# Kernel optimization log

Measured on AMD Instinct MI355X. Metric: run time of the kernel, lower is better.

Reference implementation:

```python
import jax, jax.numpy as jnp
import numpy as np

HIDDEN_DIM = 64
MEMORY_SLOTS = 8
SEQ_LEN = 24
VOCAB_SIZE = 64
B = 262144


def setup_inputs() -> dict:
    key = jax.random.key(0)
    ks = jax.random.split(key, 7)
    return {
        "seqs": jax.random.randint(ks[0], (B, SEQ_LEN), 0, VOCAB_SIZE, dtype=jnp.int64) if jax.config.jax_enable_x64 else jax.random.randint(ks[0], (B, SEQ_LEN), 0, VOCAB_SIZE, dtype=jnp.int32),
        "query_tok": jax.random.randint(ks[1], (B,), 0, VOCAB_SIZE, dtype=jnp.int32),
        "embed_W": jax.random.normal(ks[2], (VOCAB_SIZE + 2, HIDDEN_DIM), dtype=jnp.float32),
        "W1": jax.random.normal(ks[3], (HIDDEN_DIM, 2 * HIDDEN_DIM), dtype=jnp.float32) * 0.08,
        "b1": jax.random.normal(ks[4], (HIDDEN_DIM,), dtype=jnp.float32) * 0.02,
        "W2": jax.random.normal(ks[5], (VOCAB_SIZE, HIDDEN_DIM), dtype=jnp.float32) * 0.12,
        "b2": jax.random.normal(ks[6], (VOCAB_SIZE,), dtype=jnp.float32) * 0.02,
    }


def reference(seqs, query_tok, embed_W, W1, b1, W2, b2):
    # FIFO of size MEMORY_SLOTS over tokens t in [0, SEQ_LEN-1):
    # mem_summary depends only on the last MEMORY_SLOTS of those tokens.
    mem_toks = seqs[:, SEQ_LEN - 1 - MEMORY_SLOTS : SEQ_LEN - 1]      # [B, M]
    mem_summary = jnp.mean(embed_W[mem_toks], axis=1)                 # [B, H]
    q_emb = embed_W[query_tok]                                        # [B, H]
    x = jnp.concatenate([q_emb, mem_summary], axis=-1)               # [B, 2H]
    h = jax.nn.relu(x @ W1.T + b1)                                    # [B, H]
    logits = h @ W2.T + b2                                            # [B, V]
    return logits
```

## Files before the change

kernel.cpp:

```cpp
#include <hip/hip_runtime.h>


#define RSTRIDE_W 36
#define T2_OFF_W  (64 * RSTRIDE_W)
#define LDS_DW    (2 * 64 * RSTRIDE_W)

typedef __attribute__((ext_vector_type(4))) float    f32x4;
typedef __attribute__((ext_vector_type(4))) int      i32x4;
typedef __attribute__((ext_vector_type(8))) _Float16 f16x8;

__global__ void prep_kernel(const float* __restrict__ embed,
                            const float* __restrict__ W1,
                            const float* __restrict__ b1,
                            unsigned short* __restrict__ T) {
  const int t    = blockIdx.x & 63;
  const int half = blockIdx.x >> 6;
  const int j    = threadIdx.x;
  const f32x4* w4 = (const f32x4*)(W1 + j * 128 + half * 64);
  const f32x4* e4 = (const f32x4*)(embed + t * 64);
  float acc = 0.f;
#pragma unroll
  for (int k = 0; k < 16; ++k) {
    f32x4 a = w4[k], b = e4[k];
    acc += a[0] * b[0] + a[1] * b[1] + a[2] * b[2] + a[3] * b[3];
  }
  const float outv = half ? acc * 0.125f : acc + b1[j];
  ((_Float16*)T)[half * (64 * 2 * RSTRIDE_W) + t * (2 * RSTRIDE_W) + j] =
      (_Float16)outv;
}

__global__ __launch_bounds__(256, 4) void lru_kernel(
    const int*      __restrict__ seqs,
    const int*      __restrict__ qtok,
    const float*    __restrict__ W2,
    const float*    __restrict__ b2,
    const unsigned* __restrict__ T,
    float*          __restrict__ out) {
  __shared__ __align__(16) unsigned lds[LDS_DW];
  const int tid = threadIdx.x;

  {
    const uint4* src = (const uint4*)T;
    uint4*       dst = (uint4*)lds;
#pragma unroll
    for (int r = 0; r < 4; ++r) dst[tid + r * 256] = src[tid + r * 256];
    if (tid < 128) dst[tid + 1024] = src[tid + 1024];
  }

  const int lane = tid & 63;
  const int wv   = tid >> 6;
  const int qd   = lane >> 4;
  const int l15  = lane & 15;

  f16x8 bfr[4][2];
  float bb[4];
#pragma unroll
  for (int nt = 0; nt < 4; ++nt) {
    const int    row = l15 * 4 + nt;
    const float* wr  = W2 + row * 64 + qd * 8;
#pragma unroll
    for (int ks = 0; ks < 2; ++ks) {
      f32x4 w0 = *(const f32x4*)(wr + ks * 32);
      f32x4 w1 = *(const f32x4*)(wr + ks * 32 + 4);
      f16x8 f;
      f[0] = (_Float16)w0[0]; f[1] = (_Float16)w0[1];
      f[2] = (_Float16)w0[2]; f[3] = (_Float16)w0[3];
      f[4] = (_Float16)w1[0]; f[5] = (_Float16)w1[1];
      f[6] = (_Float16)w1[2]; f[7] = (_Float16)w1[3];
      bfr[nt][ks] = f;
    }
    bb[nt] = b2[row];
  }

  const int wbase  = blockIdx.x * 256 + wv * 64;
  const int myelem = wbase + lane;
  const int* srow  = seqs + myelem * 24;
  const i32x4 t0 = __builtin_nontemporal_load((const i32x4*)(srow + 12));
  const i32x4 t1 = __builtin_nontemporal_load((const i32x4*)(srow + 16));
  const i32x4 t2 = __builtin_nontemporal_load((const i32x4*)(srow + 20));
  const int   tq = __builtin_nontemporal_load(qtok + myelem);
  __syncthreads();

#pragma unroll
  for (int it = 0; it < 4; ++it) {
    const int b0  = wbase + it * 16;
    const int src = it * 16 + l15;

    const int qt = __shfl(tq, src);
    int tk[8];
    tk[0] = __shfl(t0.w, src);
    tk[1] = __shfl(t1.x, src);
    tk[2] = __shfl(t1.y, src);
    tk[3] = __shfl(t1.z, src);
    tk[4] = __shfl(t1.w, src);
    tk[5] = __shfl(t2.x, src);
    tk[6] = __shfl(t2.y, src);
    tk[7] = __shfl(t2.z, src);

    f16x8 a0, a1;
    {
      const f16x8* r1 = (const f16x8*)(lds + qt * RSTRIDE_W + qd * 4);
      a0 = r1[0];
      a1 = r1[4];
    }
#pragma unroll
    for (int s = 0; s < 8; ++s) {
      const f16x8* r2 =
          (const f16x8*)(lds + T2_OFF_W + tk[s] * RSTRIDE_W + qd * 4);
      a0 += r2[0];
      a1 += r2[4];
    }
    const f16x8 z = {(_Float16)0, (_Float16)0, (_Float16)0, (_Float16)0,
                     (_Float16)0, (_Float16)0, (_Float16)0, (_Float16)0};
    const f16x8 afA = __builtin_elementwise_max(a0, z);
    const f16x8 afB = __builtin_elementwise_max(a1, z);

    f32x4 acc[4];
#pragma unroll
    for (int nt = 0; nt < 4; ++nt) {
      f32x4 a;
      a[0] = bb[nt]; a[1] = bb[nt]; a[2] = bb[nt]; a[3] = bb[nt];
      a = __builtin_amdgcn_mfma_f32_16x16x32_f16(afA, bfr[nt][0], a, 0, 0, 0);
      a = __builtin_amdgcn_mfma_f32_16x16x32_f16(afB, bfr[nt][1], a, 0, 0, 0);
      acc[nt] = a;
    }
    float* op = out + (size_t)(b0 + qd * 4) * 64 + l15 * 4;
#pragma unroll
    for (int r = 0; r < 4; ++r) {
      f32x4 v;
      v[0] = acc[0][r]; v[1] = acc[1][r]; v[2] = acc[2][r]; v[3] = acc[3][r];
      __builtin_nontemporal_store(v, (f32x4*)(op + (size_t)r * 64));
    }
  }
}

extern "C" void kernel_launch(void* const* d_in, const int* in_sizes, int n_in,
                              void* d_out, int out_size, void* d_ws, size_t ws_size,
                              hipStream_t stream) {
  const int*   seqs  = (const int*)d_in[0];
  const int*   qtokp = (const int*)d_in[1];
  const float* embed = (const float*)d_in[2];
  const float* W1    = (const float*)d_in[3];
  const float* b1    = (const float*)d_in[4];
  const float* W2    = (const float*)d_in[5];
  const float* b2    = (const float*)d_in[6];
  float*       outp  = (float*)d_out;

  prep_kernel<<<dim3(128), dim3(64), 0, stream>>>(embed, W1, b1,
                                                  (unsigned short*)d_ws);
  lru_kernel<<<dim3(1024), dim3(256), 0, stream>>>(seqs, qtokp, W2, b2,
                                                   (const unsigned*)d_ws, outp);
}
```

Before: 113.1 us.

## Precompute fp16 W2 fragments in prep kernel and swap MFMA operand roles

Result: slower. 124.5 us (+10.1%).

```diff
diff --git a/kernel.cpp b/kernel.cpp
--- a/kernel.cpp
+++ b/kernel.cpp
@@ -4,6 +4,7 @@
 #define RSTRIDE_W 36
 #define T2_OFF_W  (64 * RSTRIDE_W)
 #define LDS_DW    (2 * 64 * RSTRIDE_W)
+#define W2F_OFF_H (128 * 2 * RSTRIDE_W)
 
 typedef __attribute__((ext_vector_type(4))) float    f32x4;
 typedef __attribute__((ext_vector_type(4))) int      i32x4;
@@ -12,27 +13,45 @@
 __global__ void prep_kernel(const float* __restrict__ embed,
                             const float* __restrict__ W1,
                             const float* __restrict__ b1,
+                            const float* __restrict__ W2,
                             unsigned short* __restrict__ T) {
-  const int t    = blockIdx.x & 63;
-  const int half = blockIdx.x >> 6;
-  const int j    = threadIdx.x;
-  const f32x4* w4 = (const f32x4*)(W1 + j * 128 + half * 64);
-  const f32x4* e4 = (const f32x4*)(embed + t * 64);
-  float acc = 0.f;
+  const int bid = blockIdx.x;
+  const int j   = threadIdx.x;
+  if (bid < 128) {
+    const int t    = bid & 63;
+    const int half = bid >> 6;
+    const f32x4* w4 = (const f32x4*)(W1 + j * 128 + half * 64);
+    const f32x4* e4 = (const f32x4*)(embed + t * 64);
+    float acc = 0.f;
 #pragma unroll
-  for (int k = 0; k < 16; ++k) {
-    f32x4 a = w4[k], b = e4[k];
-    acc += a[0] * b[0] + a[1] * b[1] + a[2] * b[2] + a[3] * b[3];
+    for (int k = 0; k < 16; ++k) {
+      f32x4 a = w4[k], b = e4[k];
+      acc += a[0] * b[0] + a[1] * b[1] + a[2] * b[2] + a[3] * b[3];
+    }
+    const float outv = half ? acc * 0.125f : acc + b1[j];
+    ((_Float16*)T)[half * (64 * 2 * RSTRIDE_W) + t * (2 * RSTRIDE_W) + j] =
+        (_Float16)outv;
+  } else {
+    const int b   = bid - 128;
+    const int nt  = b >> 1;
+    const int ks  = b & 1;
+    const int l15 = j & 15;
+    const int qd  = j >> 4;
+    const float* wr = W2 + (nt * 16 + l15) * 64 + ks * 32 + qd * 8;
+    f32x4 w0 = *(const f32x4*)(wr);
+    f32x4 w1 = *(const f32x4*)(wr + 4);
+    f16x8 f;
+    f[0] = (_Float16)w0[0]; f[1] = (_Float16)w0[1];
+    f[2] = (_Float16)w0[2]; f[3] = (_Float16)w0[3];
+    f[4] = (_Float16)w1[0]; f[5] = (_Float16)w1[1];
+    f[6] = (_Float16)w1[2]; f[7] = (_Float16)w1[3];
+    *(f16x8*)((_Float16*)T + W2F_OFF_H + (size_t)(b * 64 + j) * 8) = f;
   }
-  const float outv = half ? acc * 0.125f : acc + b1[j];
-  ((_Float16*)T)[half * (64 * 2 * RSTRIDE_W) + t * (2 * RSTRIDE_W) + j] =
-      (_Float16)outv;
 }
 
 __global__ __launch_bounds__(256, 4) void lru_kernel(
     const int*      __restrict__ seqs,
     const int*      __restrict__ qtok,
-    const float*    __restrict__ W2,
     const float*    __restrict__ b2,
     const unsigned* __restrict__ T,
     float*          __restrict__ out) {
@@ -52,24 +71,18 @@
   const int qd   = lane >> 4;
   const int l15  = lane & 15;
 
-  f16x8 bfr[4][2];
-  float bb[4];
+  f16x8 afW[4][2];
+  f32x4 bb4[4];
+  {
+    const _Float16* w2f = (const _Float16*)T + W2F_OFF_H;
 #pragma unroll
-  for (int nt = 0; nt < 4; ++nt) {
-    const int    row = l15 * 4 + nt;
-    const float* wr  = W2 + row * 64 + qd * 8;
+    for (int nt = 0; nt < 4; ++nt) {
 #pragma unroll
-    for (int ks = 0; ks < 2; ++ks) {
-      f32x4 w0 = *(const f32x4*)(wr + ks * 32);
-      f32x4 w1 = *(const f32x4*)(wr + ks * 32 + 4);
-      f16x8 f;
-      f[0] = (_Float16)w0[0]; f[1] = (_Float16)w0[1];
-      f[2] = (_Float16)w0[2]; f[3] = (_Float16)w0[3];
-      f[4] = (_Float16)w1[0]; f[5] = (_Float16)w1[1];
-      f[6] = (_Float16)w1[2]; f[7] = (_Float16)w1[3];
-      bfr[nt][ks] = f;
+      for (int ks = 0; ks < 2; ++ks)
+        afW[nt][ks] =
+            *(const f16x8*)(w2f + (size_t)(((nt << 1) | ks) * 64 + lane) * 8);
+      bb4[nt] = *(const f32x4*)(b2 + nt * 16 + qd * 4);
     }
-    bb[nt] = b2[row];
   }
 
   const int wbase  = blockIdx.x * 256 + wv * 64;
@@ -115,21 +128,13 @@
     const f16x8 afA = __builtin_elementwise_max(a0, z);
     const f16x8 afB = __builtin_elementwise_max(a1, z);
 
-    f32x4 acc[4];
+    float* op = out + (size_t)(b0 + l15) * 64 + qd * 4;
 #pragma unroll
     for (int nt = 0; nt < 4; ++nt) {
-      f32x4 a;
-      a[0] = bb[nt]; a[1] = bb[nt]; a[2] = bb[nt]; a[3] = bb[nt];
-      a = __builtin_amdgcn_mfma_f32_16x16x32_f16(afA, bfr[nt][0], a, 0, 0, 0);
-      a = __builtin_amdgcn_mfma_f32_16x16x32_f16(afB, bfr[nt][1], a, 0, 0, 0);
-      acc[nt] = a;
-    }
-    float* op = out + (size_t)(b0 + qd * 4) * 64 + l15 * 4;
-#pragma unroll
-    for (int r = 0; r < 4; ++r) {
-      f32x4 v;
-      v[0] = acc[0][r]; v[1] = acc[1][r]; v[2] = acc[2][r]; v[3] = acc[3][r];
-      __builtin_nontemporal_store(v, (f32x4*)(op + (size_t)r * 64));
+      f32x4 a = bb4[nt];
+      a = __builtin_amdgcn_mfma_f32_16x16x32_f16(afW[nt][0], afA, a, 0, 0, 0);
+      a = __builtin_amdgcn_mfma_f32_16x16x32_f16(afW[nt][1], afB, a, 0, 0, 0);
+      __builtin_nontemporal_store(a, (f32x4*)(op + nt * 16));
     }
   }
 }
@@ -146,8 +151,8 @@
   const float* b2    = (const float*)d_in[6];
   float*       outp  = (float*)d_out;
 
-  prep_kernel<<<dim3(128), dim3(64), 0, stream>>>(embed, W1, b1,
+  prep_kernel<<<dim3(136), dim3(64), 0, stream>>>(embed, W1, b1, W2,
                                                   (unsigned short*)d_ws);
-  lru_kernel<<<dim3(1024), dim3(256), 0, stream>>>(seqs, qtokp, W2, b2,
+  lru_kernel<<<dim3(1024), dim3(256), 0, stream>>>(seqs, qtokp, b2,
                                                    (const unsigned*)d_ws, outp);
 }
```

## Pack memory tokens into bytes, transpose MFMA operands, and widen prep blocks

Applied to the files above, without the earlier changes.

New measurement: 117.4 us. 3.8% more time.

```diff
diff --git a/kernel.cpp b/kernel.cpp
--- a/kernel.cpp
+++ b/kernel.cpp
@@ -13,9 +13,10 @@
                             const float* __restrict__ W1,
                             const float* __restrict__ b1,
                             unsigned short* __restrict__ T) {
-  const int t    = blockIdx.x & 63;
-  const int half = blockIdx.x >> 6;
-  const int j    = threadIdx.x;
+  const int job  = blockIdx.x * 4 + (threadIdx.x >> 6);
+  const int j    = threadIdx.x & 63;
+  const int t    = job & 63;
+  const int half = job >> 6;
   const f32x4* w4 = (const f32x4*)(W1 + j * 128 + half * 64);
   const f32x4* e4 = (const f32x4*)(embed + t * 64);
   float acc = 0.f;
@@ -52,12 +53,11 @@
   const int qd   = lane >> 4;
   const int l15  = lane & 15;
 
-  f16x8 bfr[4][2];
-  float bb[4];
+  f16x8 afW[4][2];
+  f32x4 bb4[4];
 #pragma unroll
   for (int nt = 0; nt < 4; ++nt) {
-    const int    row = l15 * 4 + nt;
-    const float* wr  = W2 + row * 64 + qd * 8;
+    const float* wr = W2 + (nt * 16 + l15) * 64 + qd * 8;
 #pragma unroll
     for (int ks = 0; ks < 2; ++ks) {
       f32x4 w0 = *(const f32x4*)(wr + ks * 32);
@@ -67,9 +67,9 @@
       f[2] = (_Float16)w0[2]; f[3] = (_Float16)w0[3];
       f[4] = (_Float16)w1[0]; f[5] = (_Float16)w1[1];
       f[6] = (_Float16)w1[2]; f[7] = (_Float16)w1[3];
-      bfr[nt][ks] = f;
+      afW[nt][ks] = f;
     }
-    bb[nt] = b2[row];
+    bb4[nt] = *(const f32x4*)(b2 + nt * 16 + qd * 4);
   }
 
   const int wbase  = blockIdx.x * 256 + wv * 64;
@@ -79,6 +79,8 @@
   const i32x4 t1 = __builtin_nontemporal_load((const i32x4*)(srow + 16));
   const i32x4 t2 = __builtin_nontemporal_load((const i32x4*)(srow + 20));
   const int   tq = __builtin_nontemporal_load(qtok + myelem);
+  const int pk0 = t0.w | (t1.x << 8) | (t1.y << 16) | (t1.z << 24);
+  const int pk1 = t1.w | (t2.x << 8) | (t2.y << 16) | (t2.z << 24);
   __syncthreads();
 
 #pragma unroll
@@ -86,16 +88,9 @@
     const int b0  = wbase + it * 16;
     const int src = it * 16 + l15;
 
-    const int qt = __shfl(tq, src);
-    int tk[8];
-    tk[0] = __shfl(t0.w, src);
-    tk[1] = __shfl(t1.x, src);
-    tk[2] = __shfl(t1.y, src);
-    tk[3] = __shfl(t1.z, src);
-    tk[4] = __shfl(t1.w, src);
-    tk[5] = __shfl(t2.x, src);
-    tk[6] = __shfl(t2.y, src);
-    tk[7] = __shfl(t2.z, src);
+    const int u0 = __shfl(pk0, src);
+    const int u1 = __shfl(pk1, src);
+    const int qt = __shfl(tq,  src);
 
     f16x8 a0, a1;
     {
@@ -104,9 +99,18 @@
       a1 = r1[4];
     }
 #pragma unroll
-    for (int s = 0; s < 8; ++s) {
+    for (int s = 0; s < 4; ++s) {
+      const int tk = (u0 >> (8 * s)) & 63;
       const f16x8* r2 =
-          (const f16x8*)(lds + T2_OFF_W + tk[s] * RSTRIDE_W + qd * 4);
+          (const f16x8*)(lds + T2_OFF_W + tk * RSTRIDE_W + qd * 4);
+      a0 += r2[0];
+      a1 += r2[4];
+    }
+#pragma unroll
+    for (int s = 0; s < 4; ++s) {
+      const int tk = (u1 >> (8 * s)) & 63;
+      const f16x8* r2 =
+          (const f16x8*)(lds + T2_OFF_W + tk * RSTRIDE_W + qd * 4);
       a0 += r2[0];
       a1 += r2[4];
     }
@@ -115,21 +119,13 @@
     const f16x8 afA = __builtin_elementwise_max(a0, z);
     const f16x8 afB = __builtin_elementwise_max(a1, z);
 
-    f32x4 acc[4];
+    float* op = out + (size_t)(b0 + l15) * 64 + qd * 4;
 #pragma unroll
     for (int nt = 0; nt < 4; ++nt) {
-      f32x4 a;
-      a[0] = bb[nt]; a[1] = bb[nt]; a[2] = bb[nt]; a[3] = bb[nt];
-      a = __builtin_amdgcn_mfma_f32_16x16x32_f16(afA, bfr[nt][0], a, 0, 0, 0);
-      a = __builtin_amdgcn_mfma_f32_16x16x32_f16(afB, bfr[nt][1], a, 0, 0, 0);
-      acc[nt] = a;
-    }
-    float* op = out + (size_t)(b0 + qd * 4) * 64 + l15 * 4;
-#pragma unroll
-    for (int r = 0; r < 4; ++r) {
-      f32x4 v;
-      v[0] = acc[0][r]; v[1] = acc[1][r]; v[2] = acc[2][r]; v[3] = acc[3][r];
-      __builtin_nontemporal_store(v, (f32x4*)(op + (size_t)r * 64));
+      f32x4 a = bb4[nt];
+      a = __builtin_amdgcn_mfma_f32_16x16x32_f16(afW[nt][0], afA, a, 0, 0, 0);
+      a = __builtin_amdgcn_mfma_f32_16x16x32_f16(afW[nt][1], afB, a, 0, 0, 0);
+      __builtin_nontemporal_store(a, (f32x4*)(op + nt * 16));
     }
   }
 }
@@ -146,7 +142,7 @@
   const float* b2    = (const float*)d_in[6];
   float*       outp  = (float*)d_out;
 
-  prep_kernel<<<dim3(128), dim3(64), 0, stream>>>(embed, W1, b1,
+  prep_kernel<<<dim3(32), dim3(256), 0, stream>>>(embed, W1, b1,
                                                   (unsigned short*)d_ws);
   lru_kernel<<<dim3(1024), dim3(256), 0, stream>>>(seqs, qtokp, W2, b2,
                                                    (const unsigned*)d_ws, outp);
```
